# Optimization experiments

Measured on AMD Instinct MI355X. Metric: run time of the kernel, lower is better.

Reference implementation:

```python
import jax, jax.numpy as jnp
import numpy as np

B, C, H, W = 4, 128, 128, 128
E, K, HID = 11, 6, 512  # num_experts, active_experts, 4*dim


def setup_inputs() -> dict:
    key = jax.random.key(0)
    ks = jax.random.split(key, 5)
    return {
        "x": jax.random.normal(ks[0], (B, C, H, W), jnp.float32),
        "gate_w": jax.random.normal(ks[1], (E, C), jnp.float32) * 0.02,
        "gate_b": jnp.zeros((E,), jnp.float32),
        "w1": jax.random.normal(ks[2], (E, HID, C), jnp.float32) * 0.02,
        "b1": jnp.zeros((E, HID), jnp.float32),
        "w2": jax.random.normal(ks[3], (E, C, HID), jnp.float32) * 0.02,
        "b2": jnp.zeros((E, C), jnp.float32),
    }


def reference(x, gate_w, gate_b, w1, b1, w2, b2):
    n_experts = gate_w.shape[0]
    k = K  # active_experts
    # channels-last for per-pixel routing / 1x1-conv-as-matmul
    xcl = jnp.transpose(x, (0, 2, 3, 1))  # [B,H,W,C]
    # --- router (1x1 conv gate + softmax over experts + top-k) ---
    logits = jnp.einsum('bhwc,ec->bhwe', xcl, gate_w) + gate_b
    scores = jax.nn.softmax(logits, axis=-1)            # [B,H,W,E]
    topk_p, topk_i = jax.lax.top_k(scores, k)           # [B,H,W,K]
    topk_p = topk_p / topk_p.sum(axis=-1, keepdims=True)
    # scatter routing weights into dense per-expert mask (indices distinct)
    onehot = jax.nn.one_hot(topk_i, n_experts, dtype=x.dtype)  # [B,H,W,K,E]
    mask = jnp.einsum('bhwke,bhwk->bhwe', onehot, topk_p)      # [B,H,W,E]
    # --- dense expert compute, masked accumulate (as in original loop) ---
    acc = jnp.zeros_like(xcl)
    for e in range(n_experts):
        h = jax.nn.gelu(jnp.einsum('bhwc,dc->bhwd', xcl, w1[e]) + b1[e],
                        approximate=False)  # torch GELU is exact erf form
        oe = jnp.einsum('bhwd,cd->bhwc', h, w2[e]) + b2[e]
        acc = acc + mask[..., e:e + 1] * oe
    y = x + jnp.transpose(acc, (0, 3, 1, 2))  # back to NCHW
    # --- load-balancing aux loss ---
    mean_prob = scores.mean(axis=(0, 1, 2))            # [E]
    mean_load = onehot.sum(axis=3).mean(axis=(0, 1, 2))  # binary mask mean, [E]
    aux_loss = n_experts * jnp.sum(mean_prob * mean_load)
    return (y, aux_loss)
```

## Files before the change

kernel.cpp:

```cpp
#include <hip/hip_runtime.h>
#include <stdint.h>

#define C_   128
#define HW_  16384
#define CHW_ (C_*HW_)
#define N_   65536
#define E_   11
#define K_   6
#define HID_ 512

typedef __attribute__((ext_vector_type(8))) _Float16 half8;
typedef __attribute__((ext_vector_type(2))) _Float16 h2;
typedef __attribute__((ext_vector_type(2))) __fp16 fp16v2;
typedef __attribute__((ext_vector_type(16))) float float16v;
typedef __attribute__((ext_vector_type(2))) unsigned uint2v;

#define GLD(g, s) __builtin_amdgcn_global_load_lds( \
    (const __attribute__((address_space(1))) unsigned int*)(uintptr_t)(g), \
    (__attribute__((address_space(3))) unsigned int*)(unsigned int)(uintptr_t)(s), 16, 0, 0)

__device__ __forceinline__ h2 pkrtz(float a, float b){
  union { fp16v2 f; h2 h; } u;
  u.f = __builtin_amdgcn_cvt_pkrtz(a, b);
  return u.h;
}
__device__ __forceinline__ h2 gelu2h(h2 v, h2 wr2){
  h2 u = v * v;
  h2 s = u * (h2)(_Float16)(-0.00076957f) + (h2)(_Float16)(0.0147811f);
  s = s * u + (h2)(_Float16)(-0.126434f);
  s = s * u + (h2)(_Float16)(0.795742f);
  h2 p = v * s;
  h2 phi = p * (h2)(_Float16)(0.5f) + (h2)(_Float16)(0.5f);
  return v * wr2 * phi;
}
__device__ __forceinline__ void pswap32(unsigned &a, unsigned &b){
#if __has_builtin(__builtin_amdgcn_permlane32_swap)
  uint2v r = __builtin_amdgcn_permlane32_swap(a, b, false, false);
  a = r.x; b = r.y;
#else
  asm volatile("v_permlane32_swap_b32 %0, %1" : "+v"(a), "+v"(b));
#endif
}

__global__ __launch_bounds__(256) void k_convert(const float* __restrict__ w1,
                                                 const float* __restrict__ w2,
                                                 const float* __restrict__ b1,
                                                 unsigned short* __restrict__ wimg,
                                                 unsigned short* __restrict__ b1h,
                                                 float* __restrict__ auxsum){
  int t = blockIdx.x * 256 + threadIdx.x;
  if (t < 23) auxsum[t] = 0.0f;
  if (t >= 185856) return;
  if (t >= 180224){
    int t2 = t - 180224;
    int rec = t2 >> 5, j5 = t2 & 31;
    int hi = j5 >> 4, j = j5 & 15;
    int e = rec >> 4, hc = rec & 15;
    int row = (j & 3) + 8 * (j >> 2) + 4 * hi;
    union { _Float16 h; unsigned short u; } cv;
    cv.h = (_Float16)b1[e * 512 + hc * 32 + row];
    b1h[rec * 32 + j5] = cv.u;
    return;
  }
  const float* src;
  size_t dst;
  if (t < 90112){
    int e = t >> 13, hid = (t >> 4) & 511, c8 = t & 15;
    src = w1 + (size_t)t * 8;
    int rec = e * 16 + (hid >> 5);
    int kc = c8 >> 1, half = c8 & 1;
    int l = (hid & 31) | (half << 5);
    dst = (size_t)rec * 8192 + kc * 512 + l * 8;
  } else {
    int u = t - 90112;
    int e = u >> 13, cc = (u >> 6) & 127, hd8 = u & 63;
    src = w2 + (size_t)u * 8;
    int rec = e * 16 + (hd8 >> 2);
    int kc2 = (hd8 >> 1) & 1, half = hd8 & 1, ct = cc >> 5;
    int l = (cc & 31) | (half << 5);
    dst = (size_t)rec * 8192 + 4096 + (ct * 2 + kc2) * 512 + l * 8;
  }
  float4 a = *(const float4*)src, b = *(const float4*)(src + 4);
  union { _Float16 h[8]; uint4 v; } u4;
  u4.h[0] = (_Float16)a.x; u4.h[1] = (_Float16)a.y;
  u4.h[2] = (_Float16)a.z; u4.h[3] = (_Float16)a.w;
  u4.h[4] = (_Float16)b.x; u4.h[5] = (_Float16)b.y;
  u4.h[6] = (_Float16)b.z; u4.h[7] = (_Float16)b.w;
  *(uint4*)(wimg + dst) = u4.v;
}

__global__ __launch_bounds__(256) void k_pre(const float* __restrict__ x,
                                             const float* __restrict__ gw,
                                             const float* __restrict__ gb,
                                             const float* __restrict__ b2,
                                             unsigned short* __restrict__ xcl,
                                             float* __restrict__ mask,
                                             float* __restrict__ auxsum){
  __shared__ __align__(16) float tt[64 * 130];
  __shared__ __align__(16) float g[E_ * C_];
  __shared__ float gbs[E_];
  __shared__ float ap[E_], al[E_];
  int tid = threadIdx.x;
  int pix0 = blockIdx.x * 64;
  int b = pix0 >> 14, hw0 = pix0 & 16383;
  const float* xb = x + (size_t)b * CHW_ + hw0;

  for (int i = tid; i < E_ * C_; i += 256) g[i] = gw[i];
  if (tid < E_) { gbs[tid] = gb[tid]; ap[tid] = 0.f; al[tid] = 0.f; }

  #pragma unroll 4
  for (int it = 0; it < 32; ++it){
    int flat = it * 256 + tid;
    int c = flat >> 6, p = flat & 63;
    tt[p * 130 + c] = xb[c * HW_ + p];
  }
  __syncthreads();
  #pragma unroll 4
  for (int it = 0; it < 16; ++it){
    int u = it * 256 + tid;
    int p = u >> 6, cc = u & 63;
    float f0 = tt[p * 130 + 2 * cc], f1 = tt[p * 130 + 2 * cc + 1];
    union { h2 h; unsigned u; } pv;
    pv.h = pkrtz(f0, f1);
    ((unsigned*)xcl)[(size_t)(pix0 + p) * 64 + cc] = pv.u;
  }

  int p = tid >> 2, t4 = tid & 3;
  float lg[E_];
  #pragma unroll
  for (int e = 0; e < E_; ++e) lg[e] = (t4 == 0) ? gbs[e] : 0.f;
  const float2* ttrow = (const float2*)(tt + p * 130 + t4 * 32);
  #pragma unroll 4
  for (int j2 = 0; j2 < 16; ++j2){
    float2 xv = ttrow[j2];
    #pragma unroll
    for (int e = 0; e < E_; ++e){
      float2 gv = *(const float2*)(g + e * C_ + t4 * 32 + j2 * 2);
      lg[e] = fmaf(xv.x, gv.x, lg[e]);
      lg[e] = fmaf(xv.y, gv.y, lg[e]);
    }
  }
  #pragma unroll
  for (int e = 0; e < E_; ++e){
    lg[e] += __shfl_xor(lg[e], 1, 64);
    lg[e] += __shfl_xor(lg[e], 2, 64);
  }
  float mx = lg[0];
  #pragma unroll
  for (int e = 1; e < E_; ++e) mx = fmaxf(mx, lg[e]);
  float pr[E_]; float s = 0.f;
  #pragma unroll
  for (int e = 0; e < E_; ++e){ pr[e] = expf(lg[e] - mx); s += pr[e]; }
  float inv = 1.0f / s;
  #pragma unroll
  for (int e = 0; e < E_; ++e) pr[e] *= inv;

  unsigned selmask = 0; float wsum = 0.f;
  for (int k = 0; k < K_; ++k){
    float bv = -1.f; int bi = 0;
    #pragma unroll
    for (int e = 0; e < E_; ++e){
      bool better = (((selmask >> e) & 1u) == 0u) && (pr[e] > bv);
      bv = better ? pr[e] : bv;
      bi = better ? e : bi;
    }
    selmask |= 1u << bi; wsum += bv;
  }
  float invw = 1.0f / wsum;
  if (t4 == 0){
    int pix = pix0 + p;
    #pragma unroll
    for (int e = 0; e < E_; ++e){
      bool sel = (selmask >> e) & 1u;
      mask[(size_t)pix * E_ + e] = sel ? pr[e] * invw : 0.f;
      atomicAdd(&ap[e], pr[e]);
      if (sel) atomicAdd(&al[e], 1.0f);
    }
  }
  __syncthreads();
  if (tid < E_){
    atomicAdd(&auxsum[tid], ap[tid]);
    atomicAdd(&auxsum[E_ + tid], al[tid]);
  }
  if (blockIdx.x == 0 && tid < 64){
    int nz = 0;
    for (int idx = tid; idx < E_ * C_; idx += 64)
      nz |= (__float_as_uint(b2[idx]) != 0u) ? 1 : 0;
    if (nz) atomicOr((int*)(auxsum + 22), 1);
  }
}

__global__ __launch_bounds__(256, 2) void k_ffn(const unsigned short* __restrict__ xcl,
                                                const unsigned short* __restrict__ wimg,
                                                const unsigned short* __restrict__ b1h,
                                                const float* __restrict__ b2,
                                                const float* __restrict__ mask,
                                                const float* __restrict__ aux,
                                                const float* __restrict__ x,
                                                float* __restrict__ y){
  __shared__ unsigned char smem[31744];
  int tid = threadIdx.x;
  int w = tid >> 6, l = tid & 63;
  int l31 = l & 31, hi = l >> 5;
  int hi4 = hi * 4;
  int pix0 = blockIdx.x * 128;
  const unsigned char* wimgB = (const unsigned char*)wimg;
  const unsigned char* b1hB  = (const unsigned char*)b1h;

  if (blockIdx.x == 0 && tid == 0){
    float s = 0.f;
    const float invN = 1.0f / (float)N_;
    for (int e = 0; e < E_; ++e)
      s += (aux[e] * invN) * (aux[E_ + e] * invN);
    y[(size_t)N_ * C_] = (float)E_ * s;
  }

  half8 Xf[8];
  {
    const unsigned short* xrow = xcl + ((size_t)(pix0 + w * 32 + l31) << 7) + hi * 8;
    #pragma unroll
    for (int kc = 0; kc < 8; ++kc)
      Xf[kc] = *(const half8*)(xrow + kc * 16);
  }

  half8 WregA[8], WregB[8];
  uint4 bhA[2], bhB[2];

  {
    const unsigned char* gs = wimgB + 8192 + w * 2048 + l * 16;
    GLD(gs, smem + w * 2048);
    GLD(gs + 1024, smem + w * 2048 + 1024);
    const unsigned char* ws0 = wimgB + l * 16;
    #pragma unroll
    for (int kc = 0; kc < 8; ++kc)
      WregA[kc] = *(const half8*)(ws0 + kc * 1024);
    bhA[0] = *(const uint4*)(b1hB + hi * 32);
    bhA[1] = *(const uint4*)(b1hB + hi * 32 + 16);
  }
  float* maskl = (float*)(smem + 17408);
  for (int idx = tid; idx < 2048; idx += 256){
    int pp = idx >> 4, ee = idx & 15;
    maskl[idx] = (ee < 11) ? mask[(size_t)(pix0 + pp) * 11 + ee] : 0.f;
  }
  __syncthreads();

  float16v facc[4];
  #pragma unroll
  for (int ct = 0; ct < 4; ++ct) facc[ct] = (float16v)0.0f;
  h2 wr2 = (h2)(_Float16)0.0f;

#define FFN_BODY(I, WCON, WLOAD, BHC, BHL)                                          \
  {                                                                                 \
    asm volatile("s_waitcnt vmcnt(10)" ::: "memory");                               \
    __builtin_amdgcn_s_barrier();                                                   \
    __builtin_amdgcn_sched_barrier(0);                                              \
    const int pf_ = ((I) + 1 <= 175) ? ((I) + 1) : 175;                             \
    {                                                                               \
      const unsigned char* gs_ = wimgB + (size_t)pf_ * 16384 + 8192 + w * 2048 + l * 16; \
      unsigned char* ld_ = smem + ((((I) + 1) & 1) << 13) + w * 2048;               \
      GLD(gs_, ld_);                                                                \
      GLD(gs_ + 1024, ld_ + 1024);                                                  \
    }                                                                               \
    {                                                                               \
      const unsigned char* ws_ = wimgB + (size_t)pf_ * 16384 + l * 16;              \
      _Pragma("unroll")                                                             \
      for (int kc_ = 0; kc_ < 8; ++kc_)                                             \
        WLOAD[kc_] = *(const half8*)(ws_ + kc_ * 1024);                             \
      const unsigned char* bp_ = b1hB + pf_ * 64 + hi * 32;                         \
      BHL[0] = *(const uint4*)(bp_);                                                \
      BHL[1] = *(const uint4*)(bp_ + 16);                                           \
    }                                                                               \
    __builtin_amdgcn_sched_barrier(0);                                              \
    if (((I) & 15) == 0){                                                           \
      float wrf_ = maskl[(w * 32 + l31) * 16 + ((I) >> 4)];                         \
      _Float16 wh_ = (_Float16)wrf_;                                                \
      wr2 = (h2){wh_, wh_};                                                         \
    }                                                                               \
    float16v hacc_ = (float16v)0.0f;                                                \
    _Pragma("unroll")                                                               \
    for (int kc_ = 0; kc_ < 8; ++kc_)                                               \
      hacc_ = __builtin_amdgcn_mfma_f32_32x32x16_f16(WCON[kc_], Xf[kc_], hacc_, 0, 0, 0); \
    union { uint4 v[2]; h2 h[8]; } bu_;                                             \
    bu_.v[0] = BHC[0]; bu_.v[1] = BHC[1];                                           \
    unsigned pd_[8];                                                                \
    _Pragma("unroll")                                                               \
    for (int k_ = 0; k_ < 8; ++k_){                                                 \
      h2 v_ = pkrtz(hacc_[2 * k_], hacc_[2 * k_ + 1]);                              \
      v_ = v_ + bu_.h[k_];                                                          \
      union { h2 h; unsigned u; } g_;                                               \
      g_.h = gelu2h(v_, wr2);                                                       \
      pd_[k_] = g_.u;                                                               \
    }                                                                               \
    pswap32(pd_[0], pd_[2]); pswap32(pd_[1], pd_[3]);                               \
    pswap32(pd_[4], pd_[6]); pswap32(pd_[5], pd_[7]);                               \
    union { unsigned u[4]; half8 s; } cv0_, cv1_;                                   \
    cv0_.u[0] = pd_[0]; cv0_.u[1] = pd_[1]; cv0_.u[2] = pd_[2]; cv0_.u[3] = pd_[3]; \
    cv1_.u[0] = pd_[4]; cv1_.u[1] = pd_[5]; cv1_.u[2] = pd_[6]; cv1_.u[3] = pd_[7]; \
    const unsigned char* wb_ = smem + (((I) & 1) << 13);                            \
    _Pragma("unroll")                                                               \
    for (int ct_ = 0; ct_ < 4; ++ct_){                                              \
      half8 a0_ = *(const half8*)(wb_ + (ct_ * 2 + 0) * 1024 + l * 16);             \
      half8 a1_ = *(const half8*)(wb_ + (ct_ * 2 + 1) * 1024 + l * 16);             \
      facc[ct_] = __builtin_amdgcn_mfma_f32_32x32x16_f16(a0_, cv0_.s, facc[ct_], 0, 0, 0); \
      facc[ct_] = __builtin_amdgcn_mfma_f32_32x32x16_f16(a1_, cv1_.s, facc[ct_], 0, 0, 0); \
    }                                                                               \
  }

  #pragma unroll 1
  for (int k = 0; k < 88; ++k){
    FFN_BODY(2 * k,     WregA, WregB, bhA, bhB);
    FFN_BODY(2 * k + 1, WregB, WregA, bhB, bhA);
  }
#undef FFN_BODY

  __syncthreads();
  float* lds_t = (float*)smem;
  float* b2t   = (float*)(smem + 25600);
  for (int idx = tid; idx < 1536; idx += 256){
    int cc = idx / 12, ee = idx - cc * 12;
    b2t[idx] = (ee < 11) ? b2[ee * 128 + cc] : 0.f;
  }
  int b2nz = ((const int*)aux)[22];

  #pragma unroll 1
  for (int h = 0; h < 4; ++h){
    __syncthreads();
    if (w == h){
      #pragma unroll
      for (int ct = 0; ct < 4; ++ct)
        #pragma unroll
        for (int r = 0; r < 16; ++r)
          lds_t[(ct * 32 + (r & 3) + 8 * (r >> 2) + hi4) * 33 + l31] = facc[ct][r];
    }
    __syncthreads();
    int c = tid >> 1, p16 = (tid & 1) << 4;
    int pixg = pix0 + h * 32 + p16;
    size_t base = (size_t)(pixg >> 14) * CHW_ + (size_t)c * HW_ + (pixg & 16383);
    float b2r[11];
    if (b2nz){
      #pragma unroll
      for (int e = 0; e < 11; ++e) b2r[e] = b2t[c * 12 + e];
    }
    #pragma unroll 2
    for (int v = 0; v < 4; ++v){
      float av[4];
      #pragma unroll
      for (int k = 0; k < 4; ++k) av[k] = lds_t[c * 33 + p16 + v * 4 + k];
      if (b2nz){
        #pragma unroll
        for (int k = 0; k < 4; ++k){
          const float* mr = maskl + (h * 32 + p16 + v * 4 + k) * 16;
          #pragma unroll
          for (int e = 0; e < 11; ++e) av[k] = fmaf(mr[e], b2r[e], av[k]);
        }
      }
      float4 xv = *(const float4*)(x + base + v * 4);
      float4 o = {av[0] + xv.x, av[1] + xv.y, av[2] + xv.z, av[3] + xv.w};
      *(float4*)(y + base + v * 4) = o;
    }
  }
}

extern "C" void kernel_launch(void* const* d_in, const int* in_sizes, int n_in,
                              void* d_out, int out_size, void* d_ws, size_t ws_size,
                              hipStream_t stream){
  const float* x  = (const float*)d_in[0];
  const float* gw = (const float*)d_in[1];
  const float* gb = (const float*)d_in[2];
  const float* w1 = (const float*)d_in[3];
  const float* b1 = (const float*)d_in[4];
  const float* w2 = (const float*)d_in[5];
  const float* b2 = (const float*)d_in[6];
  float* y = (float*)d_out;
  char* ws = (char*)d_ws;

  unsigned short* xcl  = (unsigned short*)ws;
  unsigned short* wimg = (unsigned short*)(ws + 16777216);
  float* mask   = (float*)(ws + 19660800);
  float* auxsum = (float*)(ws + 22544384);
  unsigned short* b1h  = (unsigned short*)(ws + 22544480);

  hipLaunchKernelGGL(k_convert, dim3(726),  dim3(256), 0, stream, w1, w2, b1, wimg, b1h, auxsum);
  hipLaunchKernelGGL(k_pre,     dim3(1024), dim3(256), 0, stream, x, gw, gb, b2, xcl, mask, auxsum);
  hipLaunchKernelGGL(k_ffn,     dim3(512),  dim3(256), 0, stream, xcl, wimg, b1h, b2, mask, auxsum, x, y);
}
```

Baseline: 368.0 us.

## Stage full expert weight records in LDS with 512-thread blocks and staggered start

Blocks grow to 512 threads covering 256 pixels, so each weight record staged in LDS is shared by twice as many pixels. Both the W1 and W2 halves of each record now go through LDS, replacing the per-wave register prefetch of W1, and two records are loaded per pipeline step into a 64KB double buffer. Each block starts at a different record offset (blockIdx mod 11) so concurrent blocks read different weights. The mask is read directly from global memory instead of being staged in LDS. In exchange there is more LDS traffic and LDS footprint, only 256 blocks are launched, and the output epilogue is reworked for 8 waves.

```diff
diff --git a/kernel.cpp b/kernel.cpp
--- a/kernel.cpp
+++ b/kernel.cpp
@@ -190,7 +190,7 @@
   }
 }
 
-__global__ __launch_bounds__(256, 2) void k_ffn(const unsigned short* __restrict__ xcl,
+__global__ __launch_bounds__(512, 2) void k_ffn(const unsigned short* __restrict__ xcl,
                                                 const unsigned short* __restrict__ wimg,
                                                 const unsigned short* __restrict__ b1h,
                                                 const float* __restrict__ b2,
@@ -198,12 +198,13 @@
                                                 const float* __restrict__ aux,
                                                 const float* __restrict__ x,
                                                 float* __restrict__ y){
-  __shared__ unsigned char smem[31744];
+  __shared__ unsigned char smem[65536];
   int tid = threadIdx.x;
   int w = tid >> 6, l = tid & 63;
   int l31 = l & 31, hi = l >> 5;
   int hi4 = hi * 4;
-  int pix0 = blockIdx.x * 128;
+  int pix0 = blockIdx.x * 256;
+  int off = (blockIdx.x % 11) * 16;
   const unsigned char* wimgB = (const unsigned char*)wimg;
   const unsigned char* b1hB  = (const unsigned char*)b1h;
 
@@ -223,25 +224,23 @@
       Xf[kc] = *(const half8*)(xrow + kc * 16);
   }
 
-  half8 WregA[8], WregB[8];
-  uint4 bhA[2], bhB[2];
+  uint4 bhA[4], bhB[4];
+  const size_t mrow = (size_t)(pix0 + w * 32 + l31) * 11;
 
   {
-    const unsigned char* gs = wimgB + 8192 + w * 2048 + l * 16;
-    GLD(gs, smem + w * 2048);
-    GLD(gs + 1024, smem + w * 2048 + 1024);
-    const unsigned char* ws0 = wimgB + l * 16;
-    #pragma unroll
-    for (int kc = 0; kc < 8; ++kc)
-      WregA[kc] = *(const half8*)(ws0 + kc * 1024);
-    bhA[0] = *(const uint4*)(b1hB + hi * 32);
-    bhA[1] = *(const uint4*)(b1hB + hi * 32 + 16);
-  }
-  float* maskl = (float*)(smem + 17408);
-  for (int idx = tid; idx < 2048; idx += 256){
-    int pp = idx >> 4, ee = idx & 15;
-    maskl[idx] = (ee < 11) ? mask[(size_t)(pix0 + pp) * 11 + ee] : 0.f;
-  }
+    #pragma unroll
+    for (int k = 0; k < 2; ++k){
+      int rec = off + k;
+      const unsigned char* gs = wimgB + (size_t)rec * 16384 + w * 2048 + l * 16;
+      unsigned char* dst = smem + k * 16384 + w * 2048;
+      GLD(gs, dst);
+      GLD(gs + 1024, dst + 1024);
+      const unsigned char* bp = b1hB + rec * 64 + hi * 32;
+      bhA[2 * k]     = *(const uint4*)(bp);
+      bhA[2 * k + 1] = *(const uint4*)(bp + 16);
+    }
+  }
+  float wrn = mask[mrow + (off >> 4)];
   __syncthreads();
 
   float16v facc[4];
@@ -249,39 +248,16 @@
   for (int ct = 0; ct < 4; ++ct) facc[ct] = (float16v)0.0f;
   h2 wr2 = (h2)(_Float16)0.0f;
 
-#define FFN_BODY(I, WCON, WLOAD, BHC, BHL)                                          \
+#define REC_BODY(WB, BH0, BH1)                                                      \
   {                                                                                 \
-    asm volatile("s_waitcnt vmcnt(10)" ::: "memory");                               \
-    __builtin_amdgcn_s_barrier();                                                   \
-    __builtin_amdgcn_sched_barrier(0);                                              \
-    const int pf_ = ((I) + 1 <= 175) ? ((I) + 1) : 175;                             \
-    {                                                                               \
-      const unsigned char* gs_ = wimgB + (size_t)pf_ * 16384 + 8192 + w * 2048 + l * 16; \
-      unsigned char* ld_ = smem + ((((I) + 1) & 1) << 13) + w * 2048;               \
-      GLD(gs_, ld_);                                                                \
-      GLD(gs_ + 1024, ld_ + 1024);                                                  \
-    }                                                                               \
-    {                                                                               \
-      const unsigned char* ws_ = wimgB + (size_t)pf_ * 16384 + l * 16;              \
-      _Pragma("unroll")                                                             \
-      for (int kc_ = 0; kc_ < 8; ++kc_)                                             \
-        WLOAD[kc_] = *(const half8*)(ws_ + kc_ * 1024);                             \
-      const unsigned char* bp_ = b1hB + pf_ * 64 + hi * 32;                         \
-      BHL[0] = *(const uint4*)(bp_);                                                \
-      BHL[1] = *(const uint4*)(bp_ + 16);                                           \
-    }                                                                               \
-    __builtin_amdgcn_sched_barrier(0);                                              \
-    if (((I) & 15) == 0){                                                           \
-      float wrf_ = maskl[(w * 32 + l31) * 16 + ((I) >> 4)];                         \
-      _Float16 wh_ = (_Float16)wrf_;                                                \
-      wr2 = (h2){wh_, wh_};                                                         \
-    }                                                                               \
     float16v hacc_ = (float16v)0.0f;                                                \
     _Pragma("unroll")                                                               \
-    for (int kc_ = 0; kc_ < 8; ++kc_)                                               \
-      hacc_ = __builtin_amdgcn_mfma_f32_32x32x16_f16(WCON[kc_], Xf[kc_], hacc_, 0, 0, 0); \
+    for (int kc_ = 0; kc_ < 8; ++kc_){                                              \
+      half8 a_ = *(const half8*)((WB) + kc_ * 1024 + l * 16);                       \
+      hacc_ = __builtin_amdgcn_mfma_f32_32x32x16_f16(a_, Xf[kc_], hacc_, 0, 0, 0);  \
+    }                                                                               \
     union { uint4 v[2]; h2 h[8]; } bu_;                                             \
-    bu_.v[0] = BHC[0]; bu_.v[1] = BHC[1];                                           \
+    bu_.v[0] = BH0; bu_.v[1] = BH1;                                                 \
     unsigned pd_[8];                                                                \
     _Pragma("unroll")                                                               \
     for (int k_ = 0; k_ < 8; ++k_){                                                 \
@@ -296,34 +272,66 @@
     union { unsigned u[4]; half8 s; } cv0_, cv1_;                                   \
     cv0_.u[0] = pd_[0]; cv0_.u[1] = pd_[1]; cv0_.u[2] = pd_[2]; cv0_.u[3] = pd_[3]; \
     cv1_.u[0] = pd_[4]; cv1_.u[1] = pd_[5]; cv1_.u[2] = pd_[6]; cv1_.u[3] = pd_[7]; \
-    const unsigned char* wb_ = smem + (((I) & 1) << 13);                            \
     _Pragma("unroll")                                                               \
     for (int ct_ = 0; ct_ < 4; ++ct_){                                              \
-      half8 a0_ = *(const half8*)(wb_ + (ct_ * 2 + 0) * 1024 + l * 16);             \
-      half8 a1_ = *(const half8*)(wb_ + (ct_ * 2 + 1) * 1024 + l * 16);             \
+      half8 a0_ = *(const half8*)((WB) + 8192 + (ct_ * 2 + 0) * 1024 + l * 16);     \
+      half8 a1_ = *(const half8*)((WB) + 8192 + (ct_ * 2 + 1) * 1024 + l * 16);     \
       facc[ct_] = __builtin_amdgcn_mfma_f32_32x32x16_f16(a0_, cv0_.s, facc[ct_], 0, 0, 0); \
       facc[ct_] = __builtin_amdgcn_mfma_f32_32x32x16_f16(a1_, cv1_.s, facc[ct_], 0, 0, 0); \
     }                                                                               \
   }
 
+#define SUPER_BODY(J, BHC, BHL)                                                     \
+  {                                                                                 \
+    asm volatile("s_waitcnt vmcnt(4)" ::: "memory");                                \
+    __builtin_amdgcn_s_barrier();                                                   \
+    __builtin_amdgcn_sched_barrier(0);                                              \
+         \
+    {                                                                               \
+      unsigned char* dbuf_ = smem + ((((J) + 1) & 1) << 15);                        \
+      _Pragma("unroll")                                                             \
+      for (int k_ = 0; k_ < 2; ++k_){                                               \
+        int rn_ = 2 * (J) + 2 + k_ + off; if (rn_ >= 176) rn_ -= 176;               \
+        const unsigned char* gs_ = wimgB + (size_t)rn_ * 16384 + w * 2048 + l * 16; \
+        unsigned char* dst_ = dbuf_ + k_ * 16384 + w * 2048;                        \
+        GLD(gs_, dst_);                                                             \
+        GLD(gs_ + 1024, dst_ + 1024);                                               \
+        const unsigned char* bp_ = b1hB + rn_ * 64 + hi * 32;                       \
+        BHL[2 * k_]     = *(const uint4*)(bp_);                                     \
+        BHL[2 * k_ + 1] = *(const uint4*)(bp_ + 16);                                \
+      }                                                                             \
+    }                                                                               \
+    __builtin_amdgcn_sched_barrier(0);                                              \
+    if (((J) & 7) == 0){           \
+      _Float16 wh_ = (_Float16)wrn;                                                 \
+      wr2 = (h2){wh_, wh_};                                                         \
+      int rn_ = 2 * (J) + 16 + off; if (rn_ >= 176) rn_ -= 176;                     \
+      wrn = mask[mrow + (rn_ >> 4)];                                                \
+    }                                                                               \
+    const unsigned char* wb_ = smem + (((J) & 1) << 15);                            \
+    REC_BODY(wb_, BHC[0], BHC[1]);                                                  \
+    REC_BODY(wb_ + 16384, BHC[2], BHC[3]);                                          \
+  }
+
   #pragma unroll 1
-  for (int k = 0; k < 88; ++k){
-    FFN_BODY(2 * k,     WregA, WregB, bhA, bhB);
-    FFN_BODY(2 * k + 1, WregB, WregA, bhB, bhA);
-  }
-#undef FFN_BODY
+  for (int jj = 0; jj < 44; ++jj){
+    SUPER_BODY(2 * jj,     bhA, bhB);
+    SUPER_BODY(2 * jj + 1, bhB, bhA);
+  }
+#undef SUPER_BODY
+#undef REC_BODY
 
   __syncthreads();
   float* lds_t = (float*)smem;
-  float* b2t   = (float*)(smem + 25600);
-  for (int idx = tid; idx < 1536; idx += 256){
+  float* b2t   = (float*)(smem + 17408);
+  for (int idx = tid; idx < 1536; idx += 512){
     int cc = idx / 12, ee = idx - cc * 12;
     b2t[idx] = (ee < 11) ? b2[ee * 128 + cc] : 0.f;
   }
   int b2nz = ((const int*)aux)[22];
 
   #pragma unroll 1
-  for (int h = 0; h < 4; ++h){
+  for (int h = 0; h < 8; ++h){
     __syncthreads();
     if (w == h){
       #pragma unroll
@@ -333,31 +341,26 @@
           lds_t[(ct * 32 + (r & 3) + 8 * (r >> 2) + hi4) * 33 + l31] = facc[ct][r];
     }
     __syncthreads();
-    int c = tid >> 1, p16 = (tid & 1) << 4;
-    int pixg = pix0 + h * 32 + p16;
+    int c = tid >> 2, p8 = (tid & 3) << 3;
+    int pixg = pix0 + h * 32 + p8;
     size_t base = (size_t)(pixg >> 14) * CHW_ + (size_t)c * HW_ + (pixg & 16383);
-    float b2r[11];
+    float av[8];
+    #pragma unroll
+    for (int k = 0; k < 8; ++k) av[k] = lds_t[c * 33 + p8 + k];
     if (b2nz){
       #pragma unroll
-      for (int e = 0; e < 11; ++e) b2r[e] = b2t[c * 12 + e];
-    }
-    #pragma unroll 2
-    for (int v = 0; v < 4; ++v){
-      float av[4];
-      #pragma unroll
-      for (int k = 0; k < 4; ++k) av[k] = lds_t[c * 33 + p16 + v * 4 + k];
-      if (b2nz){
+      for (int k = 0; k < 8; ++k){
+        const float* mr = mask + (size_t)(pixg + k) * 11;
         #pragma unroll
-        for (int k = 0; k < 4; ++k){
-          const float* mr = maskl + (h * 32 + p16 + v * 4 + k) * 16;
-          #pragma unroll
-          for (int e = 0; e < 11; ++e) av[k] = fmaf(mr[e], b2r[e], av[k]);
-        }
+        for (int e = 0; e < 11; ++e) av[k] = fmaf(mr[e], b2t[c * 12 + e], av[k]);
       }
-      float4 xv = *(const float4*)(x + base + v * 4);
-      float4 o = {av[0] + xv.x, av[1] + xv.y, av[2] + xv.z, av[3] + xv.w};
-      *(float4*)(y + base + v * 4) = o;
-    }
+    }
+    float4 xv0 = *(const float4*)(x + base);
+    float4 xv1 = *(const float4*)(x + base + 4);
+    float4 o0 = {av[0] + xv0.x, av[1] + xv0.y, av[2] + xv0.z, av[3] + xv0.w};
+    float4 o1 = {av[4] + xv1.x, av[5] + xv1.y, av[6] + xv1.z, av[7] + xv1.w};
+    *(float4*)(y + base) = o0;
+    *(float4*)(y + base + 4) = o1;
   }
 }
 
@@ -382,5 +385,5 @@
 
   hipLaunchKernelGGL(k_convert, dim3(726),  dim3(256), 0, stream, w1, w2, b1, wimg, b1h, auxsum);
   hipLaunchKernelGGL(k_pre,     dim3(1024), dim3(256), 0, stream, x, gw, gb, b2, xcl, mask, auxsum);
-  hipLaunchKernelGGL(k_ffn,     dim3(512),  dim3(256), 0, stream, xcl, wimg, b1h, b2, mask, auxsum, x, y);
-}
+  hipLaunchKernelGGL(k_ffn,     dim3(256),  dim3(512), 0, stream, xcl, wimg, b1h, b2, mask, auxsum, x, y);
+}
```

Measured after the change: 338.9 us. 1.09x faster.
